# Performance work log

Hardware: AMD Instinct MI355X
Metric: run time of the kernel (lower is better)

Reference implementation:

```python
import jax, jax.numpy as jnp
import numpy as np

B, T, D, H = 2, 2048, 1024, 16
DK = D // H  # 64
LN_EPS = 1e-5


def softmax_one(x, axis=-1):
    # softmax with an extra +1 in the denominator (allows 'attend to nothing')
    x = x - jax.lax.stop_gradient(jnp.max(x, axis=axis, keepdims=True))
    ex = jnp.exp(x)
    return ex / (1.0 + jnp.sum(ex, axis=axis, keepdims=True))


def setup_inputs() -> dict:
    rng = jax.random.key(0)
    ks = jax.random.split(rng, 16)
    s = 0.02  # param init scale
    return {
        "query": jax.random.normal(ks[0], (B, T, D), jnp.float32),
        "key": jax.random.normal(ks[1], (B, T, D), jnp.float32),
        "value": jax.random.normal(ks[2], (B, T, D), jnp.float32),
        "Wq": jax.random.normal(ks[3], (D, D), jnp.float32) * s,
        "bq": jnp.zeros((D,), jnp.float32),
        "Wk": jax.random.normal(ks[4], (D, D), jnp.float32) * s,
        "bk": jnp.zeros((D,), jnp.float32),
        "Wv": jax.random.normal(ks[5], (D, D), jnp.float32) * s,
        "bv": jnp.zeros((D,), jnp.float32),
        "Wo": jax.random.normal(ks[6], (D, D), jnp.float32) * s,
        "bo": jnp.zeros((D,), jnp.float32),
        "gamma": jnp.ones((D,), jnp.float32),
        "beta": jnp.zeros((D,), jnp.float32),
    }


def reference(query, key, value, Wq, bq, Wk, bk, Wv, bv, Wo, bo, gamma, beta):
    # qkv projections; torch Linear: y = x @ W.T + b
    q = (query @ Wq.T + bq).reshape(B, T, H, DK).transpose(0, 2, 1, 3)  # b h t d
    k = (key @ Wk.T + bk).reshape(B, T, H, DK).transpose(0, 2, 1, 3)
    v = (value @ Wv.T + bv).reshape(B, T, H, DK).transpose(0, 2, 1, 3)

    scores = jnp.einsum("bhqd,bhkd->bhqk", q, k) / np.sqrt(DK).astype(np.float32)
    attn = softmax_one(scores, axis=-1)  # mask=None path; dropout = identity (eval)

    x = jnp.einsum("bhqk,bhkd->bhqd", attn, v)  # [B,H,T,DK]
    x = x.transpose(0, 2, 1, 3).reshape(B, T, D)
    out = x @ Wo.T + bo

    # residual + LayerNorm
    y = query + out
    mu = jnp.mean(y, axis=-1, keepdims=True)
    var = jnp.mean(jnp.square(y - mu), axis=-1, keepdims=True)
    y = (y - mu) * jax.lax.rsqrt(var + LN_EPS) * gamma + beta
    return (y, attn)
```

## Files before the change

kernel.cpp:

```cpp
#include <hip/hip_runtime.h>
#include <hip/hip_bf16.h>
#include <math.h>

#define Bb 2
#define Tt 2048
#define Dd 1024
#define Hh 16
#define DKk 64

typedef __bf16 bf16_t;
typedef __bf16 bf16x8 __attribute__((ext_vector_type(8)));
typedef __bf16 bf16x4 __attribute__((ext_vector_type(4)));
typedef float f32x4 __attribute__((ext_vector_type(4)));

__device__ __forceinline__ void async16(const void* gsrc, void* ldst) {
  void* g = const_cast<void*>(gsrc);
  __builtin_amdgcn_global_load_lds(
      (__attribute__((address_space(1))) void*)g,
      (__attribute__((address_space(3))) void*)ldst, 16, 0, 0);
}

__device__ __forceinline__ bf16x8 cvt8(const float4 a, const float4 b) {
  bf16x8 o;
  o[0] = (bf16_t)a.x; o[1] = (bf16_t)a.y; o[2] = (bf16_t)a.z; o[3] = (bf16_t)a.w;
  o[4] = (bf16_t)b.x; o[5] = (bf16_t)b.y; o[6] = (bf16_t)b.z; o[7] = (bf16_t)b.w;
  return o;
}

#define LDSW(p, row, ch) \
  (*(const bf16x8*)((const char*)(p) + (row) * 128 + ((((ch) ^ (row)) & 7) << 4)))

#define GM 4096
#define GN 1024
#define GK 1024
#define BM2 64
#define BN2 128
#define BK2 64

__global__ __launch_bounds__(256) void gemm_qkv(
    const float* __restrict__ Aq, const float* __restrict__ Ak,
    const float* __restrict__ Av, const float* __restrict__ Wqp,
    const float* __restrict__ Wkp, const float* __restrict__ Wvp,
    const float* __restrict__ bqp, const float* __restrict__ bkp,
    const float* __restrict__ bvp, bf16_t* __restrict__ Cq,
    bf16_t* __restrict__ Ck, bf16_t* __restrict__ Cv) {
  __shared__ bf16_t As[BM2 * BK2];
  __shared__ bf16_t Bs[BN2 * BK2];
  const int z = blockIdx.z;
  const float* A = (z == 0) ? Aq : (z == 1) ? Ak : Av;
  const float* Bw = (z == 0) ? Wqp : (z == 1) ? Wkp : Wvp;
  const float* bias = (z == 0) ? bqp : (z == 1) ? bkp : bvp;

  const int tid = threadIdx.x;
  const int lane = tid & 63;
  const int w = tid >> 6;
  const int wy = w >> 1, wx = w & 1;
  const int m0 = blockIdx.y * BM2, n0 = blockIdx.x * BN2;
  const int q = lane >> 4, cc = lane & 15;
  const int srow = lane >> 3;
  const int scol = (lane & 7) * 8;

  f32x4 acc[2][4] = {};

  for (int k0 = 0; k0 < GK; k0 += BK2) {
    __syncthreads();
#pragma unroll
    for (int i = 0; i < 2; ++i) {
      const int row = w * 16 + i * 8 + srow;
      const float* ap = A + (size_t)(m0 + row) * GK + k0 + scol;
      *(bf16x8*)(As + row * BK2 + scol) =
          cvt8(*(const float4*)ap, *(const float4*)(ap + 4));
    }
#pragma unroll
    for (int i = 0; i < 4; ++i) {
      const int row = (w * 4 + i) * 8 + srow;
      const float* bp = Bw + (size_t)(n0 + row) * GK + k0 + scol;
      *(bf16x8*)(Bs + row * BK2 + scol) =
          cvt8(*(const float4*)bp, *(const float4*)(bp + 4));
    }
    __syncthreads();
#pragma unroll
    for (int kk = 0; kk < 2; ++kk) {
      bf16x8 af[2], bfr[4];
#pragma unroll
      for (int i = 0; i < 2; ++i)
        af[i] = *(const bf16x8*)(As + (wy * 32 + i * 16 + cc) * BK2 + kk * 32 + q * 8);
#pragma unroll
      for (int j = 0; j < 4; ++j)
        bfr[j] = *(const bf16x8*)(Bs + (wx * 64 + j * 16 + cc) * BK2 + kk * 32 + q * 8);
#pragma unroll
      for (int i = 0; i < 2; ++i)
#pragma unroll
        for (int j = 0; j < 4; ++j)
          acc[i][j] = __builtin_amdgcn_mfma_f32_16x16x32_bf16(af[i], bfr[j], acc[i][j], 0, 0, 0);
    }
  }

  if (z < 2) {
    bf16_t* C = z ? Ck : Cq;
#pragma unroll
    for (int j = 0; j < 4; ++j) {
      const int col = n0 + wx * 64 + j * 16 + cc;
      const float bv = bias[col];
#pragma unroll
      for (int i = 0; i < 2; ++i) {
        const int row = m0 + wy * 32 + i * 16 + q * 4;
#pragma unroll
        for (int r = 0; r < 4; ++r)
          C[(size_t)(row + r) * GN + col] = (bf16_t)(acc[i][j][r] + bv);
      }
    }
  } else {
    const int bdx = m0 >> 11;
    const int t00 = (m0 & (Tt - 1)) + wy * 32;
#pragma unroll
    for (int j = 0; j < 4; ++j) {
      const int col = n0 + wx * 64 + j * 16 + cc;
      const float bv = bias[col];
      const size_t rowbase = ((size_t)(bdx * Dd + col)) * Tt;
#pragma unroll
      for (int i = 0; i < 2; ++i) {
        const int t0 = t00 + i * 16 + q * 4;
        bf16x4 pk;
#pragma unroll
        for (int r = 0; r < 4; ++r) pk[r] = (bf16_t)(acc[i][j][r] + bv);
        *(bf16x4*)(Cv + rowbase + t0) = pk;
      }
    }
  }
}

__global__ __launch_bounds__(256) void gemm_obf16(
    const bf16_t* __restrict__ A, const float* __restrict__ Bw,
    const float* __restrict__ bias, bf16_t* __restrict__ C) {
  __shared__ bf16_t As[BM2 * BK2];
  __shared__ bf16_t Bs[BN2 * BK2];
  const int tid = threadIdx.x;
  const int lane = tid & 63;
  const int w = tid >> 6;
  const int wy = w >> 1, wx = w & 1;
  const int m0 = blockIdx.y * BM2, n0 = blockIdx.x * BN2;
  const int q = lane >> 4, cc = lane & 15;
  const int srow = lane >> 3;
  const int scol = (lane & 7) * 8;

  f32x4 acc[2][4] = {};

  for (int k0 = 0; k0 < GK; k0 += BK2) {
    __syncthreads();
#pragma unroll
    for (int i = 0; i < 2; ++i) {
      const int r0 = w * 16 + i * 8;
      async16(A + (size_t)(m0 + r0 + srow) * GK + k0 + scol, As + r0 * BK2);
    }
#pragma unroll
    for (int i = 0; i < 4; ++i) {
      const int row = (w * 4 + i) * 8 + srow;
      const float* bp = Bw + (size_t)(n0 + row) * GK + k0 + scol;
      *(bf16x8*)(Bs + row * BK2 + scol) =
          cvt8(*(const float4*)bp, *(const float4*)(bp + 4));
    }
    __syncthreads();
#pragma unroll
    for (int kk = 0; kk < 2; ++kk) {
      bf16x8 af[2], bfr[4];
#pragma unroll
      for (int i = 0; i < 2; ++i)
        af[i] = *(const bf16x8*)(As + (wy * 32 + i * 16 + cc) * BK2 + kk * 32 + q * 8);
#pragma unroll
      for (int j = 0; j < 4; ++j)
        bfr[j] = *(const bf16x8*)(Bs + (wx * 64 + j * 16 + cc) * BK2 + kk * 32 + q * 8);
#pragma unroll
      for (int i = 0; i < 2; ++i)
#pragma unroll
        for (int j = 0; j < 4; ++j)
          acc[i][j] = __builtin_amdgcn_mfma_f32_16x16x32_bf16(af[i], bfr[j], acc[i][j], 0, 0, 0);
    }
  }

#pragma unroll
  for (int j = 0; j < 4; ++j) {
    const int col = n0 + wx * 64 + j * 16 + cc;
    const float bv = bias[col];
#pragma unroll
    for (int i = 0; i < 2; ++i) {
      const int row = m0 + wy * 32 + i * 16 + q * 4;
#pragma unroll
      for (int r = 0; r < 4; ++r)
        C[(size_t)(row + r) * GN + col] = (bf16_t)(acc[i][j][r] + bv);
    }
  }
}

__global__ __launch_bounds__(256) void attn_fused(
    const bf16_t* __restrict__ Qm, const bf16_t* __restrict__ Km,
    const bf16_t* __restrict__ Vt_g,
    float* __restrict__ attn_out,
    bf16_t* __restrict__ Xb) {
  __shared__ bf16_t Qs[64 * 64];
  __shared__ bf16_t Ks[2][64 * 64];
  __shared__ bf16_t Vs[2][64 * 64];

  const int tid = threadIdx.x;
  const int lane = tid & 63;
  const int w = tid >> 6;
  const int qt = blockIdx.x, h = blockIdx.y, b = blockIdx.z;
  const int q = lane >> 4, cc = lane & 15;
  const size_t base = (size_t)b * Tt * Dd + (size_t)h * DKk;
  const size_t vbase = ((size_t)(b * Hh + h) * DKk) * Tt;
  const int srow = lane >> 3;
  const int gcol = ((lane & 7) ^ srow) * 8;
  const int l2 = lane >> 2;
  const int lc = lane & 3;
  const float CL = 0.18033688f;
  const float C2 = 11.54156028f;

#pragma unroll
  for (int i = 0; i < 2; ++i) {
    const int r0 = w * 16 + i * 8;
    async16(Qm + base + (size_t)(qt * 64 + r0 + srow) * Dd + gcol, Qs + r0 * 64);
    async16(Km + base + (size_t)(r0 + srow) * Dd + gcol, Ks[0] + r0 * 64);
  }

  float Mp[4], Lp[4];
#pragma unroll
  for (int r = 0; r < 4; ++r) { Mp[r] = -3.0e38f; Lp[r] = 0.f; }

  for (int kt = 0; kt < 32; ++kt) {
    __syncthreads();
    if (kt < 31) {
      bf16_t* kd = Ks[(kt + 1) & 1];
#pragma unroll
      for (int i = 0; i < 2; ++i) {
        const int r0 = w * 16 + i * 8;
        async16(Km + base + (size_t)((kt + 1) * 64 + r0 + srow) * Dd + gcol, kd + r0 * 64);
      }
    }
    const bf16_t* kc = Ks[kt & 1];
    f32x4 acc[4] = {};
    __builtin_amdgcn_s_setprio(1);
#pragma unroll
    for (int kk = 0; kk < 2; ++kk) {
      const bf16x8 af = LDSW(Qs, w * 16 + cc, kk * 4 + q);
#pragma unroll
      for (int j = 0; j < 4; ++j) {
        const bf16x8 bfr = LDSW(kc, j * 16 + cc, kk * 4 + q);
        acc[j] = __builtin_amdgcn_mfma_f32_16x16x32_bf16(af, bfr, acc[j], 0, 0, 0);
      }
    }
    __builtin_amdgcn_s_setprio(0);
#pragma unroll
    for (int r = 0; r < 4; ++r) {
      Mp[r] = fmaxf(Mp[r], fmaxf(fmaxf(acc[0][r], acc[1][r]),
                                 fmaxf(acc[2][r], acc[3][r])));
      Lp[r] += exp2f(fmaf(acc[0][r], CL, -C2)) + exp2f(fmaf(acc[1][r], CL, -C2)) +
               exp2f(fmaf(acc[2][r], CL, -C2)) + exp2f(fmaf(acc[3][r], CL, -C2));
    }
  }

  float inv1[4];
#pragma unroll
  for (int r = 0; r < 4; ++r) {
    float mx = Mp[r];
#pragma unroll
    for (int msk = 1; msk < 16; msk <<= 1) mx = fmaxf(mx, __shfl_xor(mx, msk));
    float ls = Lp[r];
#pragma unroll
    for (int msk = 1; msk < 16; msk <<= 1) ls += __shfl_xor(ls, msk);
    inv1[r] = 1.0f / (exp2f(fmaf(mx, CL, -C2)) + ls);
  }

#pragma unroll
  for (int i = 0; i < 2; ++i) {
    const int r0 = w * 16 + i * 8;
    async16(Km + base + (size_t)(r0 + srow) * Dd + gcol, Ks[0] + r0 * 64);
    async16(Vt_g + vbase + (size_t)(r0 + srow) * Tt + gcol, Vs[0] + r0 * 64);
  }

  f32x4 xacc[4] = {};
  const size_t arowbase = ((size_t)(b * Hh + h) * Tt + (size_t)qt * 64) * Tt;

  for (int kt = 0; kt < 32; ++kt) {
    __syncthreads();
    if (kt < 31) {
      bf16_t* kd = Ks[(kt + 1) & 1];
      bf16_t* vd = Vs[(kt + 1) & 1];
#pragma unroll
      for (int i = 0; i < 2; ++i) {
        const int r0 = w * 16 + i * 8;
        async16(Km + base + (size_t)((kt + 1) * 64 + r0 + srow) * Dd + gcol, kd + r0 * 64);
        async16(Vt_g + vbase + (size_t)(r0 + srow) * Tt + (kt + 1) * 64 + gcol, vd + r0 * 64);
      }
    }
    const bf16_t* kc = Ks[kt & 1];
    const bf16_t* vc = Vs[kt & 1];

    f32x4 acc[4] = {};
    __builtin_amdgcn_s_setprio(1);
#pragma unroll
    for (int kk = 0; kk < 2; ++kk) {
      const bf16x8 af = LDSW(Qs, w * 16 + cc, kk * 4 + q);
#pragma unroll
      for (int j = 0; j < 4; ++j) {
        const bf16x8 bfr = LDSW(kc, j * 16 + cc, kk * 4 + q);
        acc[j] = __builtin_amdgcn_mfma_f32_16x16x32_bf16(af, bfr, acc[j], 0, 0, 0);
      }
    }
    __builtin_amdgcn_s_setprio(0);

    __builtin_amdgcn_sched_barrier(0);
    __builtin_amdgcn_s_barrier();

    char* sfw = (char*)(&Ks[kt & 1][0]) + w * 2048;
#pragma unroll
    for (int half = 0; half < 2; ++half) {
#pragma unroll
      for (int jj = 0; jj < 2; ++jj) {
        const int j = half * 2 + jj;
#pragma unroll
        for (int r = 0; r < 4; ++r) {
          const int row16 = q * 4 + r;
          const float p = exp2f(fmaf(acc[j][r], CL, -C2)) * inv1[r];
          *(float*)(sfw + row16 * 128 +
                    (((jj * 16 + cc) * 4) ^ ((row16 & 7) << 4))) = p;
        }
      }
#pragma unroll
      for (int s = 0; s < 2; ++s) {
        const int ch = lc + 4 * s;
        const f32x4 v = *(const f32x4*)(sfw + l2 * 128 +
                                        ((ch * 16) ^ ((l2 & 7) << 4)));
        const int prow = w * 16 + l2;
        *(f32x4*)(attn_out + arowbase + (size_t)prow * Tt + kt * 64 +
                  half * 32 + ch * 4) = v;
      }
      const char* p0 = sfw + cc * 128;
      const f32x4 a = *(const f32x4*)(p0 + ((q * 32) ^ ((cc & 7) << 4)));
      const f32x4 bb = *(const f32x4*)(p0 + ((q * 32 + 16) ^ ((cc & 7) << 4)));
      bf16x8 af;
      af[0] = (bf16_t)a[0]; af[1] = (bf16_t)a[1];
      af[2] = (bf16_t)a[2]; af[3] = (bf16_t)a[3];
      af[4] = (bf16_t)bb[0]; af[5] = (bf16_t)bb[1];
      af[6] = (bf16_t)bb[2]; af[7] = (bf16_t)bb[3];
      __builtin_amdgcn_s_setprio(1);
#pragma unroll
      for (int j = 0; j < 4; ++j) {
        const bf16x8 bfr = LDSW(vc, j * 16 + cc, half * 4 + q);
        xacc[j] = __builtin_amdgcn_mfma_f32_16x16x32_bf16(af, bfr, xacc[j], 0, 0, 0);
      }
      __builtin_amdgcn_s_setprio(0);
    }
  }

#pragma unroll
  for (int j = 0; j < 4; ++j)
#pragma unroll
    for (int r = 0; r < 4; ++r) {
      const int row = qt * 64 + w * 16 + q * 4 + r;
      Xb[base + (size_t)row * Dd + j * 16 + cc] = (bf16_t)xacc[j][r];
    }
}

__global__ __launch_bounds__(256) void ln_kernel(
    const float* __restrict__ resid, const bf16_t* __restrict__ O,
    const float* __restrict__ gamma, const float* __restrict__ beta,
    float* __restrict__ out) {
  const int row = blockIdx.x;
  const int tid = threadIdx.x;
  const size_t roff = (size_t)row * Dd + tid * 4;
  const float4 rv = *(const float4*)(resid + roff);
  const bf16x4 ov = *(const bf16x4*)(O + roff);
  const float y0 = rv.x + (float)ov.x;
  const float y1 = rv.y + (float)ov.y;
  const float y2 = rv.z + (float)ov.z;
  const float y3 = rv.w + (float)ov.w;
  float s = y0 + y1 + y2 + y3;
  float s2 = y0 * y0 + y1 * y1 + y2 * y2 + y3 * y3;
#pragma unroll
  for (int msk = 1; msk < 64; msk <<= 1) {
    s += __shfl_xor(s, msk);
    s2 += __shfl_xor(s2, msk);
  }
  __shared__ float red[8];
  const int w = tid >> 6;
  if ((tid & 63) == 0) { red[w] = s; red[4 + w] = s2; }
  __syncthreads();
  s = red[0] + red[1] + red[2] + red[3];
  s2 = red[4] + red[5] + red[6] + red[7];
  const float mu = s * (1.f / Dd);
  const float rstd = rsqrtf(s2 * (1.f / Dd) - mu * mu + 1e-5f);
  const float4 gv = *(const float4*)(gamma + tid * 4);
  const float4 bv = *(const float4*)(beta + tid * 4);
  float4 o;
  o.x = (y0 - mu) * rstd * gv.x + bv.x;
  o.y = (y1 - mu) * rstd * gv.y + bv.y;
  o.z = (y2 - mu) * rstd * gv.z + bv.z;
  o.w = (y3 - mu) * rstd * gv.w + bv.w;
  *(float4*)(out + roff) = o;
}

extern "C" void kernel_launch(void* const* d_in, const int* in_sizes, int n_in,
                              void* d_out, int out_size, void* d_ws, size_t ws_size,
                              hipStream_t stream) {
  const float* query = (const float*)d_in[0];
  const float* key = (const float*)d_in[1];
  const float* value = (const float*)d_in[2];
  const float* Wq = (const float*)d_in[3];
  const float* bq = (const float*)d_in[4];
  const float* Wk = (const float*)d_in[5];
  const float* bk = (const float*)d_in[6];
  const float* Wv = (const float*)d_in[7];
  const float* bv = (const float*)d_in[8];
  const float* Wo = (const float*)d_in[9];
  const float* bo = (const float*)d_in[10];
  const float* gamma = (const float*)d_in[11];
  const float* beta = (const float*)d_in[12];

  float* y_out = (float*)d_out;
  float* attn_out = y_out + (size_t)Bb * Tt * Dd;

  char* p = (char*)d_ws;
  const size_t nTD = (size_t)Bb * Tt * Dd;
  bf16_t* Qb = (bf16_t*)p;  p += nTD * 2;
  bf16_t* Kb = (bf16_t*)p;  p += nTD * 2;
  bf16_t* VtG = (bf16_t*)p; p += nTD * 2;
  bf16_t* Xb = (bf16_t*)p;  p += nTD * 2;
  bf16_t* Ob = (bf16_t*)p;  p += nTD * 2;

  dim3 gqkv(GN / BN2, GM / BM2, 3);
  gemm_qkv<<<gqkv, 256, 0, stream>>>(query, key, value, Wq, Wk, Wv,
                                     bq, bk, bv, Qb, Kb, VtG);

  dim3 ga(Tt / 64, Hh, Bb);
  attn_fused<<<ga, 256, 0, stream>>>(Qb, Kb, VtG, attn_out, Xb);

  dim3 go(GN / BN2, GM / BM2);
  gemm_obf16<<<go, 256, 0, stream>>>(Xb, Wo, bo, Ob);

  ln_kernel<<<Bb * Tt, 256, 0, stream>>>(query, Ob, gamma, beta, y_out);
}
```

Baseline: 911.7 us.

## Pre-convert inputs and weights to bf16 and use async-loaded 128x128 GEMM tiles

Adds a kernel that converts the activations and all four weight matrices to bf16 once, up front. The QKV and output projection GEMMs then load both operands straight into LDS with async global-to-LDS copies and use larger 128x128 tiles. This removes repeated fp32 loads and per-tile conversion of the weights and raises data reuse per block. In exchange it adds an extra conversion pass, more workspace memory, and fewer blocks per GEMM.

```diff
diff --git a/kernel.cpp b/kernel.cpp
--- a/kernel.cpp
+++ b/kernel.cpp
@@ -30,66 +30,89 @@
 #define LDSW(p, row, ch) \
   (*(const bf16x8*)((const char*)(p) + (row) * 128 + ((((ch) ^ (row)) & 7) << 4)))
 
+__global__ __launch_bounds__(256) void cvt_all(
+    const float* __restrict__ q, const float* __restrict__ k,
+    const float* __restrict__ v, const float* __restrict__ wq,
+    const float* __restrict__ wk, const float* __restrict__ wv,
+    const float* __restrict__ wo, bf16_t* __restrict__ qb,
+    bf16_t* __restrict__ kb, bf16_t* __restrict__ vb,
+    bf16_t* __restrict__ wqb, bf16_t* __restrict__ wkb,
+    bf16_t* __restrict__ wvb, bf16_t* __restrict__ wob) {
+  const int bid = blockIdx.x;
+  const float* src;
+  bf16_t* dst;
+  size_t n;
+  int nb, b0;
+  if (bid < 768) {
+    const int t = bid >> 8;
+    b0 = bid & 255; nb = 256;
+    src = (t == 0) ? q : (t == 1) ? k : v;
+    dst = (t == 0) ? qb : (t == 1) ? kb : vb;
+    n = (size_t)Bb * Tt * Dd;
+  } else {
+    const int t = (bid - 768) >> 6;
+    b0 = (bid - 768) & 63; nb = 64;
+    src = (t == 0) ? wq : (t == 1) ? wk : (t == 2) ? wv : wo;
+    dst = (t == 0) ? wqb : (t == 1) ? wkb : (t == 2) ? wvb : wob;
+    n = (size_t)Dd * Dd;
+  }
+  const size_t stride = (size_t)nb * 256 * 8;
+  for (size_t i = ((size_t)b0 * 256 + threadIdx.x) * 8; i < n; i += stride) {
+    const float4 a = *(const float4*)(src + i);
+    const float4 b2 = *(const float4*)(src + i + 4);
+    *(bf16x8*)(dst + i) = cvt8(a, b2);
+  }
+}
+
 #define GM 4096
 #define GN 1024
 #define GK 1024
-#define BM2 64
-#define BN2 128
-#define BK2 64
-
-__global__ __launch_bounds__(256) void gemm_qkv(
-    const float* __restrict__ Aq, const float* __restrict__ Ak,
-    const float* __restrict__ Av, const float* __restrict__ Wqp,
-    const float* __restrict__ Wkp, const float* __restrict__ Wvp,
+
+__global__ __launch_bounds__(256) void gemm_qkv_bf16(
+    const bf16_t* __restrict__ Aq, const bf16_t* __restrict__ Ak,
+    const bf16_t* __restrict__ Av, const bf16_t* __restrict__ Wqb,
+    const bf16_t* __restrict__ Wkb, const bf16_t* __restrict__ Wvb,
     const float* __restrict__ bqp, const float* __restrict__ bkp,
     const float* __restrict__ bvp, bf16_t* __restrict__ Cq,
     bf16_t* __restrict__ Ck, bf16_t* __restrict__ Cv) {
-  __shared__ bf16_t As[BM2 * BK2];
-  __shared__ bf16_t Bs[BN2 * BK2];
+  __shared__ bf16_t As[128 * 64];
+  __shared__ bf16_t Bs[128 * 64];
   const int z = blockIdx.z;
-  const float* A = (z == 0) ? Aq : (z == 1) ? Ak : Av;
-  const float* Bw = (z == 0) ? Wqp : (z == 1) ? Wkp : Wvp;
+  const bf16_t* A = (z == 0) ? Aq : (z == 1) ? Ak : Av;
+  const bf16_t* Bw = (z == 0) ? Wqb : (z == 1) ? Wkb : Wvb;
   const float* bias = (z == 0) ? bqp : (z == 1) ? bkp : bvp;
 
   const int tid = threadIdx.x;
   const int lane = tid & 63;
   const int w = tid >> 6;
   const int wy = w >> 1, wx = w & 1;
-  const int m0 = blockIdx.y * BM2, n0 = blockIdx.x * BN2;
+  const int m0 = blockIdx.y * 128, n0 = blockIdx.x * 128;
   const int q = lane >> 4, cc = lane & 15;
   const int srow = lane >> 3;
   const int scol = (lane & 7) * 8;
 
-  f32x4 acc[2][4] = {};
-
-  for (int k0 = 0; k0 < GK; k0 += BK2) {
-    __syncthreads();
-#pragma unroll
-    for (int i = 0; i < 2; ++i) {
-      const int row = w * 16 + i * 8 + srow;
-      const float* ap = A + (size_t)(m0 + row) * GK + k0 + scol;
-      *(bf16x8*)(As + row * BK2 + scol) =
-          cvt8(*(const float4*)ap, *(const float4*)(ap + 4));
-    }
+  f32x4 acc[4][4] = {};
+
+  for (int k0 = 0; k0 < GK; k0 += 64) {
+    __syncthreads();
 #pragma unroll
     for (int i = 0; i < 4; ++i) {
-      const int row = (w * 4 + i) * 8 + srow;
-      const float* bp = Bw + (size_t)(n0 + row) * GK + k0 + scol;
-      *(bf16x8*)(Bs + row * BK2 + scol) =
-          cvt8(*(const float4*)bp, *(const float4*)(bp + 4));
+      const int r0 = w * 32 + i * 8;
+      async16(A + (size_t)(m0 + r0 + srow) * GK + k0 + scol, As + r0 * 64);
+      async16(Bw + (size_t)(n0 + r0 + srow) * GK + k0 + scol, Bs + r0 * 64);
     }
     __syncthreads();
 #pragma unroll
     for (int kk = 0; kk < 2; ++kk) {
-      bf16x8 af[2], bfr[4];
-#pragma unroll
-      for (int i = 0; i < 2; ++i)
-        af[i] = *(const bf16x8*)(As + (wy * 32 + i * 16 + cc) * BK2 + kk * 32 + q * 8);
+      bf16x8 af[4], bfr[4];
+#pragma unroll
+      for (int i = 0; i < 4; ++i)
+        af[i] = *(const bf16x8*)(As + (wy * 64 + i * 16 + cc) * 64 + kk * 32 + q * 8);
 #pragma unroll
       for (int j = 0; j < 4; ++j)
-        bfr[j] = *(const bf16x8*)(Bs + (wx * 64 + j * 16 + cc) * BK2 + kk * 32 + q * 8);
-#pragma unroll
-      for (int i = 0; i < 2; ++i)
+        bfr[j] = *(const bf16x8*)(Bs + (wx * 64 + j * 16 + cc) * 64 + kk * 32 + q * 8);
+#pragma unroll
+      for (int i = 0; i < 4; ++i)
 #pragma unroll
         for (int j = 0; j < 4; ++j)
           acc[i][j] = __builtin_amdgcn_mfma_f32_16x16x32_bf16(af[i], bfr[j], acc[i][j], 0, 0, 0);
@@ -103,8 +126,8 @@
       const int col = n0 + wx * 64 + j * 16 + cc;
       const float bv = bias[col];
 #pragma unroll
-      for (int i = 0; i < 2; ++i) {
-        const int row = m0 + wy * 32 + i * 16 + q * 4;
+      for (int i = 0; i < 4; ++i) {
+        const int row = m0 + wy * 64 + i * 16 + q * 4;
 #pragma unroll
         for (int r = 0; r < 4; ++r)
           C[(size_t)(row + r) * GN + col] = (bf16_t)(acc[i][j][r] + bv);
@@ -112,14 +135,14 @@
     }
   } else {
     const int bdx = m0 >> 11;
-    const int t00 = (m0 & (Tt - 1)) + wy * 32;
+    const int t00 = (m0 & (Tt - 1)) + wy * 64;
 #pragma unroll
     for (int j = 0; j < 4; ++j) {
       const int col = n0 + wx * 64 + j * 16 + cc;
       const float bv = bias[col];
       const size_t rowbase = ((size_t)(bdx * Dd + col)) * Tt;
 #pragma unroll
-      for (int i = 0; i < 2; ++i) {
+      for (int i = 0; i < 4; ++i) {
         const int t0 = t00 + i * 16 + q * 4;
         bf16x4 pk;
 #pragma unroll
@@ -130,48 +153,42 @@
   }
 }
 
-__global__ __launch_bounds__(256) void gemm_obf16(
-    const bf16_t* __restrict__ A, const float* __restrict__ Bw,
+__global__ __launch_bounds__(256) void gemm_bt_bf16(
+    const bf16_t* __restrict__ A, const bf16_t* __restrict__ Bw,
     const float* __restrict__ bias, bf16_t* __restrict__ C) {
-  __shared__ bf16_t As[BM2 * BK2];
-  __shared__ bf16_t Bs[BN2 * BK2];
+  __shared__ bf16_t As[128 * 64];
+  __shared__ bf16_t Bs[128 * 64];
   const int tid = threadIdx.x;
   const int lane = tid & 63;
   const int w = tid >> 6;
   const int wy = w >> 1, wx = w & 1;
-  const int m0 = blockIdx.y * BM2, n0 = blockIdx.x * BN2;
+  const int m0 = blockIdx.y * 128, n0 = blockIdx.x * 128;
   const int q = lane >> 4, cc = lane & 15;
   const int srow = lane >> 3;
   const int scol = (lane & 7) * 8;
 
-  f32x4 acc[2][4] = {};
-
-  for (int k0 = 0; k0 < GK; k0 += BK2) {
-    __syncthreads();
-#pragma unroll
-    for (int i = 0; i < 2; ++i) {
-      const int r0 = w * 16 + i * 8;
-      async16(A + (size_t)(m0 + r0 + srow) * GK + k0 + scol, As + r0 * BK2);
-    }
+  f32x4 acc[4][4] = {};
+
+  for (int k0 = 0; k0 < GK; k0 += 64) {
+    __syncthreads();
 #pragma unroll
     for (int i = 0; i < 4; ++i) {
-      const int row = (w * 4 + i) * 8 + srow;
-      const float* bp = Bw + (size_t)(n0 + row) * GK + k0 + scol;
-      *(bf16x8*)(Bs + row * BK2 + scol) =
-          cvt8(*(const float4*)bp, *(const float4*)(bp + 4));
+      const int r0 = w * 32 + i * 8;
+      async16(A + (size_t)(m0 + r0 + srow) * GK + k0 + scol, As + r0 * 64);
+      async16(Bw + (size_t)(n0 + r0 + srow) * GK + k0 + scol, Bs + r0 * 64);
     }
     __syncthreads();
 #pragma unroll
     for (int kk = 0; kk < 2; ++kk) {
-      bf16x8 af[2], bfr[4];
-#pragma unroll
-      for (int i = 0; i < 2; ++i)
-        af[i] = *(const bf16x8*)(As + (wy * 32 + i * 16 + cc) * BK2 + kk * 32 + q * 8);
+      bf16x8 af[4], bfr[4];
+#pragma unroll
+      for (int i = 0; i < 4; ++i)
+        af[i] = *(const bf16x8*)(As + (wy * 64 + i * 16 + cc) * 64 + kk * 32 + q * 8);
 #pragma unroll
       for (int j = 0; j < 4; ++j)
-        bfr[j] = *(const bf16x8*)(Bs + (wx * 64 + j * 16 + cc) * BK2 + kk * 32 + q * 8);
-#pragma unroll
-      for (int i = 0; i < 2; ++i)
+        bfr[j] = *(const bf16x8*)(Bs + (wx * 64 + j * 16 + cc) * 64 + kk * 32 + q * 8);
+#pragma unroll
+      for (int i = 0; i < 4; ++i)
 #pragma unroll
         for (int j = 0; j < 4; ++j)
           acc[i][j] = __builtin_amdgcn_mfma_f32_16x16x32_bf16(af[i], bfr[j], acc[i][j], 0, 0, 0);
@@ -183,8 +200,8 @@
     const int col = n0 + wx * 64 + j * 16 + cc;
     const float bv = bias[col];
 #pragma unroll
-    for (int i = 0; i < 2; ++i) {
-      const int row = m0 + wy * 32 + i * 16 + q * 4;
+    for (int i = 0; i < 4; ++i) {
+      const int row = m0 + wy * 64 + i * 16 + q * 4;
 #pragma unroll
       for (int r = 0; r < 4; ++r)
         C[(size_t)(row + r) * GN + col] = (bf16_t)(acc[i][j][r] + bv);
@@ -421,21 +438,32 @@
 
   char* p = (char*)d_ws;
   const size_t nTD = (size_t)Bb * Tt * Dd;
-  bf16_t* Qb = (bf16_t*)p;  p += nTD * 2;
-  bf16_t* Kb = (bf16_t*)p;  p += nTD * 2;
-  bf16_t* VtG = (bf16_t*)p; p += nTD * 2;
-  bf16_t* Xb = (bf16_t*)p;  p += nTD * 2;
-  bf16_t* Ob = (bf16_t*)p;  p += nTD * 2;
-
-  dim3 gqkv(GN / BN2, GM / BM2, 3);
-  gemm_qkv<<<gqkv, 256, 0, stream>>>(query, key, value, Wq, Wk, Wv,
-                                     bq, bk, bv, Qb, Kb, VtG);
+  const size_t nDD = (size_t)Dd * Dd;
+  bf16_t* Qb = (bf16_t*)p;   p += nTD * 2;
+  bf16_t* Kb = (bf16_t*)p;   p += nTD * 2;
+  bf16_t* VtG = (bf16_t*)p;  p += nTD * 2;
+  bf16_t* Xb = (bf16_t*)p;   p += nTD * 2;
+  bf16_t* Ob = (bf16_t*)p;   p += nTD * 2;
+  bf16_t* Qin = (bf16_t*)p;  p += nTD * 2;
+  bf16_t* Kin = (bf16_t*)p;  p += nTD * 2;
+  bf16_t* Vin = (bf16_t*)p;  p += nTD * 2;
+  bf16_t* Wqb = (bf16_t*)p;  p += nDD * 2;
+  bf16_t* Wkb = (bf16_t*)p;  p += nDD * 2;
+  bf16_t* Wvb = (bf16_t*)p;  p += nDD * 2;
+  bf16_t* Wob = (bf16_t*)p;  p += nDD * 2;
+
+  cvt_all<<<1024, 256, 0, stream>>>(query, key, value, Wq, Wk, Wv, Wo,
+                                    Qin, Kin, Vin, Wqb, Wkb, Wvb, Wob);
+
+  dim3 gqkv(GN / 128, GM / 128, 3);
+  gemm_qkv_bf16<<<gqkv, 256, 0, stream>>>(Qin, Kin, Vin, Wqb, Wkb, Wvb,
+                                          bq, bk, bv, Qb, Kb, VtG);
 
   dim3 ga(Tt / 64, Hh, Bb);
   attn_fused<<<ga, 256, 0, stream>>>(Qb, Kb, VtG, attn_out, Xb);
 
-  dim3 go(GN / BN2, GM / BM2);
-  gemm_obf16<<<go, 256, 0, stream>>>(Xb, Wo, bo, Ob);
+  dim3 go(GN / 128, GM / 128);
+  gemm_bt_bf16<<<go, 256, 0, stream>>>(Xb, Wob, bo, Ob);
 
   ln_kernel<<<Bb * Tt, 256, 0, stream>>>(query, Ob, gamma, beta, y_out);
 }
```

New measurement: 843.7 us. 1.08x faster.
